# Optimization experiments

Measured on AMD Instinct MI355X. Metric: run time of the kernel, lower is better.

The kernel has to match this reference:

```python
import jax, jax.numpy as jnp
import numpy as np
import math


def setup_inputs() -> dict:
    key = jax.random.key(0)
    k_x, k_q, k_k, k_v, k_o = jax.random.split(key, 5)
    B, S, D_IN, H, D_K, D_V, D_OUT = 1, 4096, 512, 8, 64, 64, 512
    # torch.rand -> uniform[0,1); scaled by 0.02 to keep softmax unsaturated
    scale = 0.02
    return {
        "x": jax.random.normal(k_x, (B, S, D_IN), dtype=jnp.float32),
        "W_q": jax.random.uniform(k_q, (H, D_IN, D_K), dtype=jnp.float32) * scale,
        "W_k": jax.random.uniform(k_k, (H, D_IN, D_K), dtype=jnp.float32) * scale,
        "W_v": jax.random.uniform(k_v, (H, D_IN, D_V), dtype=jnp.float32) * scale,
        "W_o": jax.random.uniform(k_o, (H, D_V, D_OUT), dtype=jnp.float32) * scale,
    }


def reference(x, W_q, W_k, W_v, W_o):
    # x: [B,S,d_in]; W_q/W_k: [H,d_in,d_k]; W_v: [H,d_in,d_v]; W_o: [H,d_v,d_out]
    S = x.shape[-2]
    d_key = W_k.shape[-1]
    Q = jnp.einsum('hjk,blj->bhlk', W_q, x)   # [B,H,S,d_k]
    K = jnp.einsum('hjk,blj->bhlk', W_k, x)   # [B,H,S,d_k]
    V = jnp.einsum('hjk,blj->bhlk', W_v, x)   # [B,H,S,d_v]
    # causal mask: True where masked (strict upper triangle)
    mask = jnp.triu(jnp.ones((S, S), dtype=bool), k=1)  # [S,S]
    scores = jnp.einsum('bhik,bhjk->bhij', Q, K)        # [B,H,S,S]
    scores = jnp.where(mask, -jnp.inf, scores)
    # is_scaled=True: divide by sqrt(d_key) before softmax
    weights = jax.nn.softmax(scores / math.sqrt(d_key), axis=-1)
    weights = jnp.where(mask, 0.0, weights)
    values = jnp.einsum('bhij,bhjv->bhiv', weights, V)  # [B,H,S,d_v]
    return jnp.einsum('hvk,bhlv->blk', W_o, values)     # [B,S,d_out]
```

## Files before the change

kernel.cpp:

```cpp
#include <hip/hip_runtime.h>
#include <hip/hip_bf16.h>
#include <math.h>

#define S_LEN 4096
#define NH    8

typedef __attribute__((ext_vector_type(8))) short bf16x8;
typedef __attribute__((ext_vector_type(4))) short bf16x4;
typedef __attribute__((ext_vector_type(4))) float f32x4;

#define QSCALE 0.18033688011112042f

__device__ __forceinline__ short f2bf(float f) {
    union { float f; unsigned u; } v; v.f = f;
    unsigned r = v.u + 0x7fffu + ((v.u >> 16) & 1u);
    return (short)(r >> 16);
}

__device__ __forceinline__ int pk2(float a, float b) {
    __hip_bfloat162 t = __float22bfloat162_rn(make_float2(a, b));
    union { __hip_bfloat162 h; int i; } u; u.h = t;
    return u.i;
}

__device__ __forceinline__ void gload16(const void* g, void* l) {
    __builtin_amdgcn_global_load_lds(
        (const __attribute__((address_space(1))) unsigned*)g,
        (__attribute__((address_space(3))) unsigned*)l, 16, 0, 0);
}

__device__ __forceinline__ void stage_tile(const short* gsrc, size_t gstride,
                                           short* tile, int t)
{
    const int wave = t >> 6, lane = t & 63;
    const int sub = lane >> 3;
    const int cg  = (lane & 7) ^ sub;
#pragma unroll
    for (int j = 0; j < 2; ++j) {
        const int chunk = wave * 2 + j;
        const int row = chunk * 8 + sub;
        gload16(gsrc + (size_t)row * gstride + cg * 8, tile + chunk * 512);
    }
}

__device__ __forceinline__ bf16x8 frag(const short* tile, int row, int cg) {
    return *(const bf16x8*)&tile[row * 64 + ((cg ^ (row & 7)) << 3)];
}

__device__ __forceinline__ void gemm_mainloop_512(
    const short* __restrict__ Arow, const short* __restrict__ Brow,
    short* As, short* Bs, f32x4 acc[4], int t)
{
    const int wave = t >> 6, lane = t & 63, n16 = lane & 15, quad = lane >> 4;
    stage_tile(Arow, 512, As, t);
    stage_tile(Brow, 512, Bs, t);
    __syncthreads();
    for (int c = 0; c < 8; ++c) {
        const int cur = c & 1;
        if (c < 7) {
            stage_tile(Arow + (c + 1) * 64, 512, As + (1 - cur) * 4096, t);
            stage_tile(Brow + (c + 1) * 64, 512, Bs + (1 - cur) * 4096, t);
        }
        const short* as = As + cur * 4096;
        const short* bs = Bs + cur * 4096;
#pragma unroll
        for (int kh = 0; kh < 2; ++kh) {
            const bf16x8 a = frag(as, wave * 16 + n16, kh * 4 + quad);
#pragma unroll
            for (int nt = 0; nt < 4; ++nt) {
                const bf16x8 b = frag(bs, nt * 16 + n16, kh * 4 + quad);
                acc[nt] = __builtin_amdgcn_mfma_f32_16x16x32_bf16(a, b, acc[nt], 0, 0, 0);
            }
        }
        __syncthreads();
    }
}

__global__ __launch_bounds__(256) void prep_kernel(
    const float* __restrict__ x,
    const float* __restrict__ Wq, const float* __restrict__ Wk,
    const float* __restrict__ Wv, const float* __restrict__ Wo,
    short* __restrict__ xb, short* __restrict__ Wqkvt, short* __restrict__ Wot)
{
    __shared__ short T[64 * 66];
    const int b = blockIdx.x, t = threadIdx.x;
    if (b < 1024) {
        const size_t idx = (size_t)b * 2048 + t * 8;
        const float4 a = *(const float4*)&x[idx];
        const float4 c = *(const float4*)&x[idx + 4];
        bf16x8 o;
        o[0] = f2bf(a.x); o[1] = f2bf(a.y); o[2] = f2bf(a.z); o[3] = f2bf(a.w);
        o[4] = f2bf(c.x); o[5] = f2bf(c.y); o[6] = f2bf(c.z); o[7] = f2bf(c.w);
        *(bf16x8*)&xb[idx] = o;
        return;
    }
    const int c4 = (t & 15) * 4, rsub = t >> 4;
    const int orow = t >> 2, oc16 = (t & 3) * 16;
    if (b < 1216) {
        const int jj = b - 1024, g = jj >> 3, kb = jj & 7;
        const int which = g >> 3, h = g & 7;
        const float* W = ((which == 0) ? Wq : (which == 1) ? Wk : Wv) + (size_t)h * 512 * 64;
#pragma unroll
        for (int p = 0; p < 4; ++p) {
            const int row = p * 16 + rsub;
            const float4 v = *(const float4*)&W[(size_t)(kb * 64 + row) * 64 + c4];
            T[(c4 + 0) * 66 + row] = f2bf(v.x);
            T[(c4 + 1) * 66 + row] = f2bf(v.y);
            T[(c4 + 2) * 66 + row] = f2bf(v.z);
            T[(c4 + 3) * 66 + row] = f2bf(v.w);
        }
        __syncthreads();
        short* O = &Wqkvt[((size_t)g * 64 + orow) * 512 + kb * 64];
        *(bf16x8*)&O[oc16]     = *(const bf16x8*)&T[orow * 66 + oc16];
        *(bf16x8*)&O[oc16 + 8] = *(const bf16x8*)&T[orow * 66 + oc16 + 8];
    } else {
        const int jj = b - 1216, h = jj >> 3, nb = jj & 7;
        const float* W = Wo + (size_t)h * 64 * 512;
#pragma unroll
        for (int p = 0; p < 4; ++p) {
            const int row = p * 16 + rsub;
            const float4 v = *(const float4*)&W[(size_t)row * 512 + nb * 64 + c4];
            T[(c4 + 0) * 66 + row] = f2bf(v.x);
            T[(c4 + 1) * 66 + row] = f2bf(v.y);
            T[(c4 + 2) * 66 + row] = f2bf(v.z);
            T[(c4 + 3) * 66 + row] = f2bf(v.w);
        }
        __syncthreads();
        short* O = &Wot[((size_t)nb * 64 + orow) * 512 + h * 64];
        *(bf16x8*)&O[oc16]     = *(const bf16x8*)&T[orow * 66 + oc16];
        *(bf16x8*)&O[oc16 + 8] = *(const bf16x8*)&T[orow * 66 + oc16 + 8];
    }
}

__global__ __launch_bounds__(256) void qkv_gemm_kernel(
    const short* __restrict__ xb, const short* __restrict__ Wqkvt,
    short* __restrict__ Qg, short* __restrict__ Kg, short* __restrict__ Vtg)
{
    __shared__ short smem[16384];
    short* As = smem;
    short* Bs = smem + 8192;
    const int sblk = blockIdx.x, g = blockIdx.y;
    const int which = g >> 3, h = g & 7;
    const int t = threadIdx.x;
    const int wave = t >> 6, lane = t & 63, n16 = lane & 15, quad = lane >> 4;

    f32x4 acc[4] = {{0,0,0,0},{0,0,0,0},{0,0,0,0},{0,0,0,0}};
    gemm_mainloop_512(xb + (size_t)sblk * 64 * 512, Wqkvt + (size_t)g * 64 * 512,
                      As, Bs, acc, t);

    if (which < 2) {
        const float scale = (which == 0) ? QSCALE : 1.0f;
        short* O = ((which == 0) ? Qg : Kg) + (size_t)h * S_LEN * 64;
#pragma unroll
        for (int nt = 0; nt < 4; ++nt)
#pragma unroll
            for (int r = 0; r < 4; ++r) {
                const int s = sblk * 64 + wave * 16 + quad * 4 + r;
                O[(size_t)s * 64 + nt * 16 + n16] = f2bf(acc[nt][r] * scale);
            }
    } else {
        __syncthreads();
        short* Tr = smem;
#pragma unroll
        for (int nt = 0; nt < 4; ++nt)
#pragma unroll
            for (int r = 0; r < 4; ++r)
                Tr[(nt * 16 + n16) * 66 + wave * 16 + quad * 4 + r] = f2bf(acc[nt][r]);
        __syncthreads();
        short* O = Vtg + (size_t)h * 64 * S_LEN + sblk * 64;
        const int r4 = t >> 2, c16 = (t & 3) * 16;
        *(bf16x8*)&O[(size_t)r4 * S_LEN + c16]     = *(const bf16x8*)&Tr[r4 * 66 + c16];
        *(bf16x8*)&O[(size_t)r4 * S_LEN + c16 + 8] = *(const bf16x8*)&Tr[r4 * 66 + c16 + 8];
    }
}

__global__ __launch_bounds__(256) void out_gemm_kernel(
    const short* __restrict__ vals, const short* __restrict__ Wot, float* __restrict__ out)
{
    __shared__ short smem[16384];
    short* As = smem;
    short* Bs = smem + 8192;
    const int sblk = blockIdx.x, g = blockIdx.y;
    const int t = threadIdx.x;
    const int wave = t >> 6, lane = t & 63, n16 = lane & 15, quad = lane >> 4;

    f32x4 acc[4] = {{0,0,0,0},{0,0,0,0},{0,0,0,0},{0,0,0,0}};
    gemm_mainloop_512(vals + (size_t)sblk * 64 * 512, Wot + (size_t)g * 64 * 512,
                      As, Bs, acc, t);

#pragma unroll
    for (int nt = 0; nt < 4; ++nt)
#pragma unroll
        for (int r = 0; r < 4; ++r) {
            const int s = sblk * 64 + wave * 16 + quad * 4 + r;
            out[(size_t)s * 512 + g * 64 + nt * 16 + n16] = acc[nt][r];
        }
}

__global__ __launch_bounds__(256, 4) void attn_kernel(
    const short* __restrict__ Qg, const short* __restrict__ Kg,
    const short* __restrict__ Vtg, float* __restrict__ Opart, float* __restrict__ Lpart)
{
    __shared__ short Ks[2][4096];
    __shared__ short Vs[2][4096];
    __shared__ short Ps[4096];

    const int id = blockIdx.x;
    const int h  = id & 7;
    const int c  = 159 - (id >> 3);
    int qb, j;
    if (c < 16)      { qb = c;                    j = 0; }
    else if (c < 48) { qb = 16 + ((c - 16) >> 1); j = (c - 16) & 1; }
    else if (c < 96) { qb = 32 + (c - 48) / 3;    j = (c - 48) % 3; }
    else             { qb = 48 + ((c - 96) >> 2); j = (c - 96) & 3; }
    const int k0   = j * 16;
    const int kend = min(k0 + 16, qb + 1);

    const short* Kh  = Kg  + (size_t)h * S_LEN * 64;
    const short* Vth = Vtg + (size_t)h * 64 * S_LEN;

    const int t = threadIdx.x;
    const int wave = t >> 6, lane = t & 63, n16 = lane & 15, quad = lane >> 4;
    const int qrow = wave * 16 + n16;
    const int sw   = (qrow & 7) << 3;

    const short* Qr = Qg + (size_t)h * S_LEN * 64 + (size_t)(qb * 64 + qrow) * 64;
    const bf16x8 bq0 = *(const bf16x8*)&Qr[quad * 8];
    const bf16x8 bq1 = *(const bf16x8*)&Qr[32 + quad * 8];

    bf16x8 ones;
#pragma unroll
    for (int i = 0; i < 8; ++i) ones[i] = (short)0x3F80;

    f32x4 oacc[4] = {{0,0,0,0},{0,0,0,0},{0,0,0,0},{0,0,0,0}};
    f32x4 lacc = {0, 0, 0, 0};

    stage_tile(Kh + (size_t)k0 * 64 * 64, 64, Ks[0], t);
    stage_tile(Vth + k0 * 64, S_LEN, Vs[0], t);
    __syncthreads();

    for (int kb = k0; kb < kend; ++kb) {
        const int cur = (kb - k0) & 1;
        if (kb + 1 < kend) {
            stage_tile(Kh + (size_t)(kb + 1) * 64 * 64, 64, Ks[1 - cur], t);
            stage_tile(Vth + (kb + 1) * 64, S_LEN, Vs[1 - cur], t);
        }

        f32x4 sc[4] = {{0,0,0,0},{0,0,0,0},{0,0,0,0},{0,0,0,0}};
#pragma unroll
        for (int kh = 0; kh < 2; ++kh) {
            const bf16x8 bq = kh ? bq1 : bq0;
#pragma unroll
            for (int mt = 0; mt < 4; ++mt) {
                const bf16x8 a = frag(Ks[cur], mt * 16 + n16, kh * 4 + quad);
                sc[mt] = __builtin_amdgcn_mfma_f32_16x16x32_bf16(a, bq, sc[mt], 0, 0, 0);
            }
        }

        if (kb == qb) {
#pragma unroll
            for (int mt = 0; mt < 4; ++mt) {
                const int key0 = mt * 16 + quad * 4;
#pragma unroll
                for (int r = 0; r < 4; ++r)
                    if (key0 + r > qrow) sc[mt][r] = -1e30f;
            }
        }

#pragma unroll
        for (int mt = 0; mt < 4; ++mt) {
            const float p0 = __builtin_amdgcn_exp2f(sc[mt][0]);
            const float p1 = __builtin_amdgcn_exp2f(sc[mt][1]);
            const float p2 = __builtin_amdgcn_exp2f(sc[mt][2]);
            const float p3 = __builtin_amdgcn_exp2f(sc[mt][3]);
            int2 pk; pk.x = pk2(p0, p1); pk.y = pk2(p2, p3);
            *(int2*)&Ps[qrow * 64 + ((mt * 16 + quad * 4) ^ sw)] = pk;
        }
        __builtin_amdgcn_wave_barrier();

#pragma unroll
        for (int kh = 0; kh < 2; ++kh) {
            const bf16x8 bp = *(const bf16x8*)&Ps[qrow * 64 + ((kh * 32 + quad * 8) ^ sw)];
            lacc = __builtin_amdgcn_mfma_f32_16x16x32_bf16(ones, bp, lacc, 0, 0, 0);
#pragma unroll
            for (int mt = 0; mt < 4; ++mt) {
                const bf16x8 a = frag(Vs[cur], mt * 16 + n16, kh * 4 + quad);
                oacc[mt] = __builtin_amdgcn_mfma_f32_16x16x32_bf16(a, bp, oacc[mt], 0, 0, 0);
            }
        }
        __builtin_amdgcn_wave_barrier();
        __syncthreads();
    }

    float* tileO = Opart + ((size_t)(h * 160 + c) << 12);
    float* tileL = Lpart + ((h * 160 + c) << 6);
    if (quad == 0) tileL[qrow] = lacc[0];
#pragma unroll
    for (int mt = 0; mt < 4; ++mt)
#pragma unroll
        for (int r = 0; r < 4; ++r)
            tileO[((mt * 16 + quad * 4 + r) << 6) + qrow] = oacc[mt][r];
}

__global__ __launch_bounds__(256) void combine_norm_kernel(
    const float* __restrict__ Opart, const float* __restrict__ Lpart,
    short* __restrict__ vals)
{
    __shared__ short T[64 * 66];
    const int id = blockIdx.x;
    const int h = id & 7, qb = id >> 3;
    const int nj = (qb >> 4) + 1;
    int c0;
    if (qb < 16)      c0 = qb;
    else if (qb < 32) c0 = 16 + 2 * (qb - 16);
    else if (qb < 48) c0 = 48 + 3 * (qb - 32);
    else              c0 = 96 + 4 * (qb - 48);
    const int base = h * 160 + c0;

    const int t = threadIdx.x;
    const int q0 = (t & 15) * 4;
    const int vr = t >> 4;

    f32x4 L = {0, 0, 0, 0};
    for (int j = 0; j < nj; ++j)
        L += *(const f32x4*)&Lpart[((base + j) << 6) + q0];
    const f32x4 inv = {1.f / L[0], 1.f / L[1], 1.f / L[2], 1.f / L[3]};

#pragma unroll
    for (int pass = 0; pass < 4; ++pass) {
        const int v = vr + pass * 16;
        f32x4 s = {0, 0, 0, 0};
        for (int j = 0; j < nj; ++j)
            s += *(const f32x4*)&Opart[((size_t)(base + j) << 12) + (v << 6) + q0];
        T[(q0 + 0) * 66 + v] = f2bf(s[0] * inv[0]);
        T[(q0 + 1) * 66 + v] = f2bf(s[1] * inv[1]);
        T[(q0 + 2) * 66 + v] = f2bf(s[2] * inv[2]);
        T[(q0 + 3) * 66 + v] = f2bf(s[3] * inv[3]);
    }
    __syncthreads();
    const int q = t >> 2, vs = (t & 3) * 16;
    const size_t row = (size_t)(qb * 64 + q) * 512 + h * 64 + vs;
    *(bf16x8*)&vals[row]     = *(const bf16x8*)&T[q * 66 + vs];
    *(bf16x8*)&vals[row + 8] = *(const bf16x8*)&T[q * 66 + vs + 8];
}

extern "C" void kernel_launch(void* const* d_in, const int* in_sizes, int n_in,
                              void* d_out, int out_size, void* d_ws, size_t ws_size,
                              hipStream_t stream)
{
    const float* x  = (const float*)d_in[0];
    const float* Wq = (const float*)d_in[1];
    const float* Wk = (const float*)d_in[2];
    const float* Wv = (const float*)d_in[3];
    const float* Wo = (const float*)d_in[4];
    float* out = (float*)d_out;

    short* xb    = (short*)d_ws;
    short* Wqkvt = xb + 2097152;
    short* Wot   = Wqkvt + 786432;
    short* Qg    = Wot + 262144;
    short* Kg    = Qg + 2097152;
    short* Vtg   = Kg + 2097152;
    short* vals  = Vtg + 2097152;
    float* Opart = (float*)(vals + 2097152);
    float* Lpart = Opart + (size_t)1280 * 4096;

    prep_kernel<<<1280, 256, 0, stream>>>(x, Wq, Wk, Wv, Wo, xb, Wqkvt, Wot);
    qkv_gemm_kernel<<<dim3(64, 24), 256, 0, stream>>>(xb, Wqkvt, Qg, Kg, Vtg);
    attn_kernel<<<1280, 256, 0, stream>>>(Qg, Kg, Vtg, Opart, Lpart);
    combine_norm_kernel<<<512, 256, 0, stream>>>(Opart, Lpart, vals);
    out_gemm_kernel<<<dim3(64, 8), 256, 0, stream>>>(vals, Wot, out);
}
```

Measured before the change: 134.8 us.

## Use 128-row query tiles with 32x32x16 MFMA in attention

The attention kernel now gives each wave 32 query rows (128 per block) and uses 32x32x16 bf16 MFMA instead of 16x16x32. Each staged K/V tile is therefore reused across twice as many queries, halving the block count and K/V traffic. The row-sum is now done with scalar adds plus a cross-half shuffle instead of a ones-matrix MFMA, and the P buffer is padded per wave to avoid bank conflicts. The cost is more registers and lower occupancy (launch bounds 3), masking applied across two key blocks, and a combine kernel reworked for the new partition layout.

```diff
diff --git a/kernel.cpp b/kernel.cpp
--- a/kernel.cpp
+++ b/kernel.cpp
@@ -8,6 +8,7 @@
 typedef __attribute__((ext_vector_type(8))) short bf16x8;
 typedef __attribute__((ext_vector_type(4))) short bf16x4;
 typedef __attribute__((ext_vector_type(4))) float f32x4;
+typedef __attribute__((ext_vector_type(16))) float f32x16;
 
 #define QSCALE 0.18033688011112042f
 
@@ -197,43 +198,43 @@
         }
 }
 
-__global__ __launch_bounds__(256, 4) void attn_kernel(
+__global__ __launch_bounds__(256, 3) void attn_kernel(
     const short* __restrict__ Qg, const short* __restrict__ Kg,
     const short* __restrict__ Vtg, float* __restrict__ Opart, float* __restrict__ Lpart)
 {
     __shared__ short Ks[2][4096];
     __shared__ short Vs[2][4096];
-    __shared__ short Ps[4096];
+    __shared__ short Ps[4 * 32 * 72];
 
     const int id = blockIdx.x;
     const int h  = id & 7;
-    const int c  = 159 - (id >> 3);
-    int qb, j;
-    if (c < 16)      { qb = c;                    j = 0; }
-    else if (c < 48) { qb = 16 + ((c - 16) >> 1); j = (c - 16) & 1; }
-    else if (c < 96) { qb = 32 + (c - 48) / 3;    j = (c - 48) % 3; }
-    else             { qb = 48 + ((c - 96) >> 2); j = (c - 96) & 3; }
+    const int c  = 79 - (id >> 3);
+    int qs, j;
+    if (c < 8)       { qs = c;                   j = 0; }
+    else if (c < 24) { qs = 8 + ((c - 8) >> 1);  j = (c - 8) & 1; }
+    else if (c < 48) { qs = 16 + (c - 24) / 3;   j = (c - 24) % 3; }
+    else             { qs = 24 + ((c - 48) >> 2); j = (c - 48) & 3; }
     const int k0   = j * 16;
-    const int kend = min(k0 + 16, qb + 1);
+    const int kend = min(k0 + 16, 2 * qs + 2);
 
     const short* Kh  = Kg  + (size_t)h * S_LEN * 64;
     const short* Vth = Vtg + (size_t)h * 64 * S_LEN;
 
     const int t = threadIdx.x;
-    const int wave = t >> 6, lane = t & 63, n16 = lane & 15, quad = lane >> 4;
-    const int qrow = wave * 16 + n16;
-    const int sw   = (qrow & 7) << 3;
-
-    const short* Qr = Qg + (size_t)h * S_LEN * 64 + (size_t)(qb * 64 + qrow) * 64;
-    const bf16x8 bq0 = *(const bf16x8*)&Qr[quad * 8];
-    const bf16x8 bq1 = *(const bf16x8*)&Qr[32 + quad * 8];
-
-    bf16x8 ones;
-#pragma unroll
-    for (int i = 0; i < 8; ++i) ones[i] = (short)0x3F80;
-
-    f32x4 oacc[4] = {{0,0,0,0},{0,0,0,0},{0,0,0,0},{0,0,0,0}};
-    f32x4 lacc = {0, 0, 0, 0};
+    const int wave = t >> 6, lane = t & 63, l31 = lane & 31, half = lane >> 5;
+    const int qg = qs * 128 + wave * 32 + l31;
+
+    const short* Qr = Qg + (size_t)h * S_LEN * 64 + (size_t)qg * 64;
+    bf16x8 bq[4];
+#pragma unroll
+    for (int kc = 0; kc < 4; ++kc)
+        bq[kc] = *(const bf16x8*)&Qr[kc * 16 + half * 8];
+
+    f32x16 oacc[2];
+#pragma unroll
+    for (int r = 0; r < 16; ++r) { oacc[0][r] = 0.f; oacc[1][r] = 0.f; }
+    float lsum = 0.f;
+    short* Pw = Ps + wave * (32 * 72);
 
     stage_tile(Kh + (size_t)k0 * 64 * 64, 64, Ks[0], t);
     stage_tile(Vth + k0 * 64, S_LEN, Vs[0], t);
@@ -246,102 +247,107 @@
             stage_tile(Vth + (kb + 1) * 64, S_LEN, Vs[1 - cur], t);
         }
 
-        f32x4 sc[4] = {{0,0,0,0},{0,0,0,0},{0,0,0,0},{0,0,0,0}};
-#pragma unroll
-        for (int kh = 0; kh < 2; ++kh) {
-            const bf16x8 bq = kh ? bq1 : bq0;
-#pragma unroll
-            for (int mt = 0; mt < 4; ++mt) {
-                const bf16x8 a = frag(Ks[cur], mt * 16 + n16, kh * 4 + quad);
-                sc[mt] = __builtin_amdgcn_mfma_f32_16x16x32_bf16(a, bq, sc[mt], 0, 0, 0);
+        f32x16 sc[2];
+#pragma unroll
+        for (int r = 0; r < 16; ++r) { sc[0][r] = 0.f; sc[1][r] = 0.f; }
+#pragma unroll
+        for (int kc = 0; kc < 4; ++kc) {
+            const bf16x8 a0 = frag(Ks[cur], l31,      kc * 2 + half);
+            const bf16x8 a1 = frag(Ks[cur], 32 + l31, kc * 2 + half);
+            sc[0] = __builtin_amdgcn_mfma_f32_32x32x16_bf16(a0, bq[kc], sc[0], 0, 0, 0);
+            sc[1] = __builtin_amdgcn_mfma_f32_32x32x16_bf16(a1, bq[kc], sc[1], 0, 0, 0);
+        }
+
+        if (kb * 64 + 63 > qg) {
+#pragma unroll
+            for (int mt = 0; mt < 2; ++mt)
+#pragma unroll
+                for (int r = 0; r < 16; ++r) {
+                    const int key = kb * 64 + mt * 32 + (r & 3) + 8 * (r >> 2) + 4 * half;
+                    if (key > qg) sc[mt][r] = -1e30f;
+                }
+        }
+
+#pragma unroll
+        for (int mt = 0; mt < 2; ++mt)
+#pragma unroll
+            for (int g2 = 0; g2 < 4; ++g2) {
+                const float p0 = __builtin_amdgcn_exp2f(sc[mt][4 * g2 + 0]);
+                const float p1 = __builtin_amdgcn_exp2f(sc[mt][4 * g2 + 1]);
+                const float p2 = __builtin_amdgcn_exp2f(sc[mt][4 * g2 + 2]);
+                const float p3 = __builtin_amdgcn_exp2f(sc[mt][4 * g2 + 3]);
+                lsum += (p0 + p1) + (p2 + p3);
+                int2 w; w.x = pk2(p0, p1); w.y = pk2(p2, p3);
+                *(int2*)&Pw[l31 * 72 + mt * 32 + g2 * 8 + half * 4] = w;
             }
-        }
-
-        if (kb == qb) {
-#pragma unroll
-            for (int mt = 0; mt < 4; ++mt) {
-                const int key0 = mt * 16 + quad * 4;
-#pragma unroll
-                for (int r = 0; r < 4; ++r)
-                    if (key0 + r > qrow) sc[mt][r] = -1e30f;
-            }
-        }
-
-#pragma unroll
-        for (int mt = 0; mt < 4; ++mt) {
-            const float p0 = __builtin_amdgcn_exp2f(sc[mt][0]);
-            const float p1 = __builtin_amdgcn_exp2f(sc[mt][1]);
-            const float p2 = __builtin_amdgcn_exp2f(sc[mt][2]);
-            const float p3 = __builtin_amdgcn_exp2f(sc[mt][3]);
-            int2 pk; pk.x = pk2(p0, p1); pk.y = pk2(p2, p3);
-            *(int2*)&Ps[qrow * 64 + ((mt * 16 + quad * 4) ^ sw)] = pk;
-        }
         __builtin_amdgcn_wave_barrier();
 
 #pragma unroll
-        for (int kh = 0; kh < 2; ++kh) {
-            const bf16x8 bp = *(const bf16x8*)&Ps[qrow * 64 + ((kh * 32 + quad * 8) ^ sw)];
-            lacc = __builtin_amdgcn_mfma_f32_16x16x32_bf16(ones, bp, lacc, 0, 0, 0);
-#pragma unroll
-            for (int mt = 0; mt < 4; ++mt) {
-                const bf16x8 a = frag(Vs[cur], mt * 16 + n16, kh * 4 + quad);
-                oacc[mt] = __builtin_amdgcn_mfma_f32_16x16x32_bf16(a, bp, oacc[mt], 0, 0, 0);
-            }
+        for (int kc = 0; kc < 4; ++kc) {
+            const bf16x8 bp = *(const bf16x8*)&Pw[l31 * 72 + kc * 16 + half * 8];
+            const bf16x8 a0 = frag(Vs[cur], l31,      kc * 2 + half);
+            const bf16x8 a1 = frag(Vs[cur], 32 + l31, kc * 2 + half);
+            oacc[0] = __builtin_amdgcn_mfma_f32_32x32x16_bf16(a0, bp, oacc[0], 0, 0, 0);
+            oacc[1] = __builtin_amdgcn_mfma_f32_32x32x16_bf16(a1, bp, oacc[1], 0, 0, 0);
         }
         __builtin_amdgcn_wave_barrier();
         __syncthreads();
     }
 
-    float* tileO = Opart + ((size_t)(h * 160 + c) << 12);
-    float* tileL = Lpart + ((h * 160 + c) << 6);
-    if (quad == 0) tileL[qrow] = lacc[0];
-#pragma unroll
-    for (int mt = 0; mt < 4; ++mt)
-#pragma unroll
-        for (int r = 0; r < 4; ++r)
-            tileO[((mt * 16 + quad * 4 + r) << 6) + qrow] = oacc[mt][r];
+    lsum += __shfl_xor(lsum, 32);
+
+    float* tileO = Opart + (size_t)(h * 80 + c) * (64 * 128);
+    float* tileL = Lpart + (h * 80 + c) * 128;
+    if (half == 0) tileL[wave * 32 + l31] = lsum;
+#pragma unroll
+    for (int mt = 0; mt < 2; ++mt)
+#pragma unroll
+        for (int r = 0; r < 16; ++r) {
+            const int v = mt * 32 + (r & 3) + 8 * (r >> 2) + 4 * half;
+            tileO[(v << 7) + wave * 32 + l31] = oacc[mt][r];
+        }
 }
 
 __global__ __launch_bounds__(256) void combine_norm_kernel(
     const float* __restrict__ Opart, const float* __restrict__ Lpart,
     short* __restrict__ vals)
 {
-    __shared__ short T[64 * 66];
+    __shared__ short T[128 * 66];
     const int id = blockIdx.x;
-    const int h = id & 7, qb = id >> 3;
-    const int nj = (qb >> 4) + 1;
-    int c0;
-    if (qb < 16)      c0 = qb;
-    else if (qb < 32) c0 = 16 + 2 * (qb - 16);
-    else if (qb < 48) c0 = 48 + 3 * (qb - 32);
-    else              c0 = 96 + 4 * (qb - 48);
-    const int base = h * 160 + c0;
+    const int h = id & 7, qs = id >> 3;
+    int c0, nj;
+    if (qs < 8)       { c0 = qs;                nj = 1; }
+    else if (qs < 16) { c0 = 8 + 2 * (qs - 8);  nj = 2; }
+    else if (qs < 24) { c0 = 24 + 3 * (qs - 16); nj = 3; }
+    else              { c0 = 48 + 4 * (qs - 24); nj = 4; }
+    const int base = h * 80 + c0;
 
     const int t = threadIdx.x;
-    const int q0 = (t & 15) * 4;
-    const int vr = t >> 4;
+    const int q0 = (t & 31) * 4;
+    const int vr = t >> 5;
 
     f32x4 L = {0, 0, 0, 0};
     for (int j = 0; j < nj; ++j)
-        L += *(const f32x4*)&Lpart[((base + j) << 6) + q0];
+        L += *(const f32x4*)&Lpart[(base + j) * 128 + q0];
     const f32x4 inv = {1.f / L[0], 1.f / L[1], 1.f / L[2], 1.f / L[3]};
 
 #pragma unroll
-    for (int pass = 0; pass < 4; ++pass) {
-        const int v = vr + pass * 16;
+    for (int pass = 0; pass < 8; ++pass) {
+        const int v = vr + pass * 8;
         f32x4 s = {0, 0, 0, 0};
         for (int j = 0; j < nj; ++j)
-            s += *(const f32x4*)&Opart[((size_t)(base + j) << 12) + (v << 6) + q0];
+            s += *(const f32x4*)&Opart[(size_t)(base + j) * 8192 + (v << 7) + q0];
         T[(q0 + 0) * 66 + v] = f2bf(s[0] * inv[0]);
         T[(q0 + 1) * 66 + v] = f2bf(s[1] * inv[1]);
         T[(q0 + 2) * 66 + v] = f2bf(s[2] * inv[2]);
         T[(q0 + 3) * 66 + v] = f2bf(s[3] * inv[3]);
     }
     __syncthreads();
-    const int q = t >> 2, vs = (t & 3) * 16;
-    const size_t row = (size_t)(qb * 64 + q) * 512 + h * 64 + vs;
-    *(bf16x8*)&vals[row]     = *(const bf16x8*)&T[q * 66 + vs];
-    *(bf16x8*)&vals[row + 8] = *(const bf16x8*)&T[q * 66 + vs + 8];
+    const int q = t >> 1, vh = (t & 1) * 32;
+    const size_t row = (size_t)(qs * 128 + q) * 512 + h * 64 + vh;
+#pragma unroll
+    for (int u = 0; u < 4; ++u)
+        *(bf16x8*)&vals[row + u * 8] = *(const bf16x8*)&T[q * 66 + vh + u * 8];
 }
 
 extern "C" void kernel_launch(void* const* d_in, const int* in_sizes, int n_in,
@@ -363,11 +369,11 @@
     short* Vtg   = Kg + 2097152;
     short* vals  = Vtg + 2097152;
     float* Opart = (float*)(vals + 2097152);
-    float* Lpart = Opart + (size_t)1280 * 4096;
+    float* Lpart = Opart + (size_t)640 * 8192;
 
     prep_kernel<<<1280, 256, 0, stream>>>(x, Wq, Wk, Wv, Wo, xb, Wqkvt, Wot);
     qkv_gemm_kernel<<<dim3(64, 24), 256, 0, stream>>>(xb, Wqkvt, Qg, Kg, Vtg);
-    attn_kernel<<<1280, 256, 0, stream>>>(Qg, Kg, Vtg, Opart, Lpart);
-    combine_norm_kernel<<<512, 256, 0, stream>>>(Opart, Lpart, vals);
+    attn_kernel<<<640, 256, 0, stream>>>(Qg, Kg, Vtg, Opart, Lpart);
+    combine_norm_kernel<<<256, 256, 0, stream>>>(Opart, Lpart, vals);
     out_gemm_kernel<<<dim3(64, 8), 256, 0, stream>>>(vals, Wot, out);
 }
```

New measurement: 137.6 us. +2.0%, slower.
